# Kernel optimization log

Hardware: AMD Instinct MI355X
Metric: run time of the kernel (lower is better)

The kernel has to match this reference:

```python
import jax, jax.numpy as jnp
import numpy as np

STRICT_MAXIMA_BONUS = 10.0
FINAL_ADJUSTMENT = 0.0


def setup_inputs() -> dict:
    key = jax.random.key(0)
    x = jax.random.normal(key, (2, 8, 4, 256, 384), dtype=jnp.float32)
    return {"x": x}


def _conv_quad_interp3d(x, bonus, adj):
    B, C, D, H, W = x.shape
    # replicate ('edge') padding of 1 voxel, as kornia spatial_gradient3d does
    xp = jnp.pad(x, ((0, 0), (0, 0), (1, 1), (1, 1), (1, 1)), mode='edge')

    def f(dd, dh, dw):  # shifted view: value at (d+dd, h+dh, w+dw)
        return xp[:, :, 1 + dd:1 + dd + D, 1 + dh:1 + dh + H, 1 + dw:1 + dw + W]

    # first-order gradients (kornia diff kernels; depth kernel is flipped -> ds has sign of f(d-1)-f(d+1))
    b0 = 0.5 * (f(0, 0, 1) - f(0, 0, -1))   # dx
    b1 = 0.5 * (f(0, 1, 0) - f(0, -1, 0))   # dy
    b2 = 0.5 * (f(-1, 0, 0) - f(1, 0, 0))   # ds (flipped depth)

    # second-order (Hessian) entries; mixed terms carry the caller's 0.25 factor
    dxx = f(0, 0, 1) - 2.0 * x + f(0, 0, -1)
    dyy = f(0, 1, 0) - 2.0 * x + f(0, -1, 0)
    dss = f(1, 0, 0) - 2.0 * x + f(-1, 0, 0)
    dxy = 0.25 * (f(0, -1, -1) - f(0, -1, 1) - f(0, 1, -1) + f(0, 1, 1))
    dys = 0.25 * (-f(-1, -1, 0) + f(-1, 1, 0) + f(1, -1, 0) - f(1, 1, 0))  # depth-flipped
    dxs = 0.25 * (-f(-1, 0, -1) + f(-1, 0, 1) + f(1, 0, -1) - f(1, 0, 1))  # depth-flipped

    # 3x3x3 NMS mask (max-pool with -inf padding, equality with center)
    mx = jax.lax.reduce_window(x, -jnp.inf, jax.lax.max,
                               (1, 1, 3, 3, 3), (1, 1, 1, 1, 1), 'SAME')
    nms = x == mx

    # closed-form symmetric 3x3 solve: Hes @ u = b via adjugate / det
    # Hes = [[dxx,dxy,dxs],[dxy,dyy,dys],[dxs,dys,dss]]
    c00 = dyy * dss - dys * dys
    c01 = dxs * dys - dxy * dss
    c02 = dxy * dys - dxs * dyy
    c11 = dxx * dss - dxs * dxs
    c12 = dxy * dxs - dxx * dys
    c22 = dxx * dyy - dxy * dxy
    det = dxx * c00 + dxy * c01 + dxs * c02
    ok = nms & (det != 0)                       # new_nms_mask (solved correctly)
    invdet = 1.0 / jnp.where(det == 0, 1.0, det)
    u0 = (c00 * b0 + c01 * b1 + c02 * b2) * invdet
    u1 = (c01 * b0 + c11 * b1 + c12 * b2) * invdet
    u2 = (c02 * b0 + c12 * b1 + c22 * b2) * invdet

    # dx = -x_solved, only at valid NMS positions
    d0 = jnp.where(ok, -u0, 0.0)
    d1 = jnp.where(ok, -u1, 0.0)
    d2 = jnp.where(ok, -u2, 0.0)
    # zero out offsets with max-abs component > 0.7
    small = jnp.maximum(jnp.maximum(jnp.abs(d0), jnp.abs(d1)), jnp.abs(d2)) <= 0.7
    d0 = jnp.where(small, d0, 0.0)
    d1 = jnp.where(small, d1, 0.0)
    d2 = jnp.where(small, d2, 0.0)

    # quadratic value refinement dy = 0.5 * b^T dx, plus strict-maxima bonus
    dE = 0.5 * (b0 * d0 + b1 * d1 + b2 * d2)
    y_max = x + dE + bonus * ok.astype(x.dtype)

    # coords: grid channels are (d, x=w, y=h); dx_res after flip+swap_xy is (s, x, y),
    # with final_adjustment added to the x,y channels
    gd = jnp.arange(D, dtype=x.dtype)[:, None, None]
    gw = jnp.arange(W, dtype=x.dtype)[None, None, :]
    gh = jnp.arange(H, dtype=x.dtype)[None, :, None]
    coords_max = jnp.stack([gd + d2, gw + (d0 + adj), gh + (d1 + adj)], axis=2)  # (B,C,3,D,H,W)
    return coords_max, y_max


def reference(x):
    return _conv_quad_interp3d(x, STRICT_MAXIMA_BONUS, FINAL_ADJUSTMENT)
```

## Files before the change

kernel.cpp:

```cpp
#include <hip/hip_runtime.h>

#define BB 2
#define CC 8
#define DD 4
#define HH 256
#define WW 384
#define WV 4
#define WT (WW / WV)

__global__ __launch_bounds__(256) void cqi3d_kernel(const float* __restrict__ x,
                                                    float* __restrict__ coords,
                                                    float* __restrict__ ymax) {
    const int tid = blockIdx.x * blockDim.x + threadIdx.x;
    const int nthreads = BB * CC * HH * WT;
    if (tid >= nthreads) return;

    const int wt = tid % WT;
    int t = tid / WT;
    const int h = t % HH;
    const int bc = t / HH;

    const int w0 = wt * WV;

    const int hm = h > 0 ? h - 1 : 0;
    const int hp = h < HH - 1 ? h + 1 : HH - 1;
    const int hr[3] = {hm, h, hp};
    const int wl = w0 > 0 ? w0 - 1 : 0;
    const int wr = (w0 + WV < WW) ? w0 + WV : WW - 1;

    float rb[DD][3][WV + 2];
#pragma unroll
    for (int p = 0; p < DD; ++p) {
#pragma unroll
        for (int j = 0; j < 3; ++j) {
            const float* row = x + (((size_t)bc * DD + p) * HH + hr[j]) * WW;
            const float4 v4 = *reinterpret_cast<const float4*>(row + w0);
            rb[p][j][1] = v4.x;
            rb[p][j][2] = v4.y;
            rb[p][j][3] = v4.z;
            rb[p][j][4] = v4.w;
            rb[p][j][0] = row[wl];
            rb[p][j][5] = row[wr];
        }
    }

    float vm[DD][WV + 2];
#pragma unroll
    for (int p = 0; p < DD; ++p)
#pragma unroll
        for (int xx = 0; xx < WV + 2; ++xx)
            vm[p][xx] = fmaxf(fmaxf(rb[p][0][xx], rb[p][1][xx]), rb[p][2][xx]);

    const size_t plane = (size_t)HH * WW;

#pragma unroll
    for (int d = 0; d < DD; ++d) {
        const int i0 = d > 0 ? d - 1 : 0;
        const int i1 = d;
        const int i2 = d < DD - 1 ? d + 1 : DD - 1;

        float dm[WV + 2];
#pragma unroll
        for (int xx = 0; xx < WV + 2; ++xx)
            dm[xx] = fmaxf(fmaxf(vm[i0][xx], vm[i1][xx]), vm[i2][xx]);

        float yv[WV], o0[WV], o1[WV], o2[WV];
#pragma unroll
        for (int kk = 0; kk < WV; ++kk) {
            const int q = kk + 1;
            const float c = rb[i1][1][q];

            const float b0 = 0.5f * (rb[i1][1][q + 1] - rb[i1][1][q - 1]);
            const float b1 = 0.5f * (rb[i1][2][q] - rb[i1][0][q]);
            const float b2 = 0.5f * (rb[i0][1][q] - rb[i2][1][q]);

            const float dxx = rb[i1][1][q + 1] - 2.0f * c + rb[i1][1][q - 1];
            const float dyy = rb[i1][2][q] - 2.0f * c + rb[i1][0][q];
            const float dss = rb[i2][1][q] - 2.0f * c + rb[i0][1][q];
            const float dxy = 0.25f * (rb[i1][0][q - 1] - rb[i1][0][q + 1] -
                                       rb[i1][2][q - 1] + rb[i1][2][q + 1]);
            const float dys = 0.25f * (-rb[i0][0][q] + rb[i0][2][q] +
                                       rb[i2][0][q] - rb[i2][2][q]);
            const float dxs = 0.25f * (-rb[i0][1][q - 1] + rb[i0][1][q + 1] +
                                       rb[i2][1][q - 1] - rb[i2][1][q + 1]);

            const float mx = fmaxf(fmaxf(dm[q - 1], dm[q]), dm[q + 1]);
            const bool nms = (c == mx);

            const float c00 = dyy * dss - dys * dys;
            const float c01 = dxs * dys - dxy * dss;
            const float c02 = dxy * dys - dxs * dyy;
            const float c11 = dxx * dss - dxs * dxs;
            const float c12 = dxy * dxs - dxx * dys;
            const float c22 = dxx * dyy - dxy * dxy;
            const float det = dxx * c00 + dxy * c01 + dxs * c02;

            const bool ok = nms && (det != 0.0f);
            const float invdet = 1.0f / (det == 0.0f ? 1.0f : det);
            const float u0 = (c00 * b0 + c01 * b1 + c02 * b2) * invdet;
            const float u1 = (c01 * b0 + c11 * b1 + c12 * b2) * invdet;
            const float u2 = (c02 * b0 + c12 * b1 + c22 * b2) * invdet;

            float d0 = ok ? -u0 : 0.0f;
            float d1 = ok ? -u1 : 0.0f;
            float d2 = ok ? -u2 : 0.0f;

            const bool small = fmaxf(fmaxf(fabsf(d0), fabsf(d1)), fabsf(d2)) <= 0.7f;
            if (!small) { d0 = 0.0f; d1 = 0.0f; d2 = 0.0f; }

            const float dE = 0.5f * (b0 * d0 + b1 * d1 + b2 * d2);
            yv[kk] = c + dE + (ok ? 10.0f : 0.0f);
            o2[kk] = (float)d + d2;
            o0[kk] = (float)(w0 + kk) + d0;
            o1[kk] = (float)h + d1;
        }

        const size_t ybase = (((size_t)bc * DD + d) * HH + h) * WW + w0;
        *reinterpret_cast<float4*>(ymax + ybase) = make_float4(yv[0], yv[1], yv[2], yv[3]);

        const size_t cbase = (((size_t)bc * 3) * DD + d) * plane + (size_t)h * WW + w0;
        *reinterpret_cast<float4*>(coords + cbase) =
            make_float4(o2[0], o2[1], o2[2], o2[3]);
        *reinterpret_cast<float4*>(coords + cbase + DD * plane) =
            make_float4(o0[0], o0[1], o0[2], o0[3]);
        *reinterpret_cast<float4*>(coords + cbase + 2 * DD * plane) =
            make_float4(o1[0], o1[1], o1[2], o1[3]);
    }
}

extern "C" void kernel_launch(void* const* d_in, const int* in_sizes, int n_in,
                              void* d_out, int out_size, void* d_ws, size_t ws_size,
                              hipStream_t stream) {
    const float* x = (const float*)d_in[0];
    float* out = (float*)d_out;
    float* coords = out;
    float* ymax = out + (size_t)BB * CC * 3 * DD * HH * WW;

    const int nthreads = BB * CC * HH * WT;
    const int block = 256;
    const int grid = (nthreads + block - 1) / block;
    cqi3d_kernel<<<grid, block, 0, stream>>>(x, coords, ymax);
}
```

Before: 28.34 us.

## Split depth across threads and use nontemporal vector stores

Each thread now handles one depth slice instead of looping over all four, so the launch has four times as many threads, each loading only the three neighbouring depth planes. This cuts per-thread register use and raises parallelism, in exchange for reloading overlapping planes (9 row loads per output slice instead of 12 shared across 4 slices). Output stores become nontemporal vector stores so the write-only outputs bypass cache retention.

```diff
diff --git a/kernel.cpp b/kernel.cpp
--- a/kernel.cpp
+++ b/kernel.cpp
@@ -8,124 +8,119 @@
 #define WV 4
 #define WT (WW / WV)
 
+typedef float f32x4 __attribute__((ext_vector_type(4)));
+
 __global__ __launch_bounds__(256) void cqi3d_kernel(const float* __restrict__ x,
                                                     float* __restrict__ coords,
                                                     float* __restrict__ ymax) {
     const int tid = blockIdx.x * blockDim.x + threadIdx.x;
-    const int nthreads = BB * CC * HH * WT;
+    const int nthreads = BB * CC * DD * HH * WT;
     if (tid >= nthreads) return;
 
     const int wt = tid % WT;
     int t = tid / WT;
     const int h = t % HH;
-    const int bc = t / HH;
+    t /= HH;
+    const int d = t % DD;
+    const int bc = t / DD;
 
     const int w0 = wt * WV;
 
     const int hm = h > 0 ? h - 1 : 0;
     const int hp = h < HH - 1 ? h + 1 : HH - 1;
     const int hr[3] = {hm, h, hp};
+    const int dpl[3] = {d > 0 ? d - 1 : 0, d, d < DD - 1 ? d + 1 : DD - 1};
     const int wl = w0 > 0 ? w0 - 1 : 0;
     const int wr = (w0 + WV < WW) ? w0 + WV : WW - 1;
 
-    float rb[DD][3][WV + 2];
+    float rb[3][3][WV + 2];
 #pragma unroll
-    for (int p = 0; p < DD; ++p) {
+    for (int i = 0; i < 3; ++i) {
 #pragma unroll
         for (int j = 0; j < 3; ++j) {
-            const float* row = x + (((size_t)bc * DD + p) * HH + hr[j]) * WW;
-            const float4 v4 = *reinterpret_cast<const float4*>(row + w0);
-            rb[p][j][1] = v4.x;
-            rb[p][j][2] = v4.y;
-            rb[p][j][3] = v4.z;
-            rb[p][j][4] = v4.w;
-            rb[p][j][0] = row[wl];
-            rb[p][j][5] = row[wr];
+            const float* row = x + (((size_t)bc * DD + dpl[i]) * HH + hr[j]) * WW;
+            const f32x4 v4 = *reinterpret_cast<const f32x4*>(row + w0);
+            rb[i][j][1] = v4.x;
+            rb[i][j][2] = v4.y;
+            rb[i][j][3] = v4.z;
+            rb[i][j][4] = v4.w;
+            rb[i][j][0] = row[wl];
+            rb[i][j][5] = row[wr];
         }
     }
 
-    float vm[DD][WV + 2];
+    float dm[WV + 2];
 #pragma unroll
-    for (int p = 0; p < DD; ++p)
+    for (int xx = 0; xx < WV + 2; ++xx) {
+        const float m0 = fmaxf(fmaxf(rb[0][0][xx], rb[0][1][xx]), rb[0][2][xx]);
+        const float m1 = fmaxf(fmaxf(rb[1][0][xx], rb[1][1][xx]), rb[1][2][xx]);
+        const float m2 = fmaxf(fmaxf(rb[2][0][xx], rb[2][1][xx]), rb[2][2][xx]);
+        dm[xx] = fmaxf(fmaxf(m0, m1), m2);
+    }
+
+    float yv[WV], o0[WV], o1[WV], o2[WV];
 #pragma unroll
-        for (int xx = 0; xx < WV + 2; ++xx)
-            vm[p][xx] = fmaxf(fmaxf(rb[p][0][xx], rb[p][1][xx]), rb[p][2][xx]);
+    for (int kk = 0; kk < WV; ++kk) {
+        const int q = kk + 1;
+        const float c = rb[1][1][q];
+
+        const float b0 = 0.5f * (rb[1][1][q + 1] - rb[1][1][q - 1]);
+        const float b1 = 0.5f * (rb[1][2][q] - rb[1][0][q]);
+        const float b2 = 0.5f * (rb[0][1][q] - rb[2][1][q]);
+
+        const float dxx = rb[1][1][q + 1] - 2.0f * c + rb[1][1][q - 1];
+        const float dyy = rb[1][2][q] - 2.0f * c + rb[1][0][q];
+        const float dss = rb[2][1][q] - 2.0f * c + rb[0][1][q];
+        const float dxy = 0.25f * (rb[1][0][q - 1] - rb[1][0][q + 1] -
+                                   rb[1][2][q - 1] + rb[1][2][q + 1]);
+        const float dys = 0.25f * (-rb[0][0][q] + rb[0][2][q] +
+                                   rb[2][0][q] - rb[2][2][q]);
+        const float dxs = 0.25f * (-rb[0][1][q - 1] + rb[0][1][q + 1] +
+                                   rb[2][1][q - 1] - rb[2][1][q + 1]);
+
+        const float mx = fmaxf(fmaxf(dm[q - 1], dm[q]), dm[q + 1]);
+        const bool nms = (c == mx);
+
+        const float c00 = dyy * dss - dys * dys;
+        const float c01 = dxs * dys - dxy * dss;
+        const float c02 = dxy * dys - dxs * dyy;
+        const float c11 = dxx * dss - dxs * dxs;
+        const float c12 = dxy * dxs - dxx * dys;
+        const float c22 = dxx * dyy - dxy * dxy;
+        const float det = dxx * c00 + dxy * c01 + dxs * c02;
+
+        const bool ok = nms && (det != 0.0f);
+        const float invdet = 1.0f / (det == 0.0f ? 1.0f : det);
+        const float u0 = (c00 * b0 + c01 * b1 + c02 * b2) * invdet;
+        const float u1 = (c01 * b0 + c11 * b1 + c12 * b2) * invdet;
+        const float u2 = (c02 * b0 + c12 * b1 + c22 * b2) * invdet;
+
+        float d0 = ok ? -u0 : 0.0f;
+        float d1 = ok ? -u1 : 0.0f;
+        float d2 = ok ? -u2 : 0.0f;
+
+        const bool small = fmaxf(fmaxf(fabsf(d0), fabsf(d1)), fabsf(d2)) <= 0.7f;
+        if (!small) { d0 = 0.0f; d1 = 0.0f; d2 = 0.0f; }
+
+        const float dE = 0.5f * (b0 * d0 + b1 * d1 + b2 * d2);
+        yv[kk] = c + dE + (ok ? 10.0f : 0.0f);
+        o2[kk] = (float)d + d2;
+        o0[kk] = (float)(w0 + kk) + d0;
+        o1[kk] = (float)h + d1;
+    }
 
     const size_t plane = (size_t)HH * WW;
+    const size_t ybase = (((size_t)bc * DD + d) * HH + h) * WW + w0;
+    const f32x4 yq = {yv[0], yv[1], yv[2], yv[3]};
+    __builtin_nontemporal_store(yq, reinterpret_cast<f32x4*>(ymax + ybase));
 
-#pragma unroll
-    for (int d = 0; d < DD; ++d) {
-        const int i0 = d > 0 ? d - 1 : 0;
-        const int i1 = d;
-        const int i2 = d < DD - 1 ? d + 1 : DD - 1;
-
-        float dm[WV + 2];
-#pragma unroll
-        for (int xx = 0; xx < WV + 2; ++xx)
-            dm[xx] = fmaxf(fmaxf(vm[i0][xx], vm[i1][xx]), vm[i2][xx]);
-
-        float yv[WV], o0[WV], o1[WV], o2[WV];
-#pragma unroll
-        for (int kk = 0; kk < WV; ++kk) {
-            const int q = kk + 1;
-            const float c = rb[i1][1][q];
-
-            const float b0 = 0.5f * (rb[i1][1][q + 1] - rb[i1][1][q - 1]);
-            const float b1 = 0.5f * (rb[i1][2][q] - rb[i1][0][q]);
-            const float b2 = 0.5f * (rb[i0][1][q] - rb[i2][1][q]);
-
-            const float dxx = rb[i1][1][q + 1] - 2.0f * c + rb[i1][1][q - 1];
-            const float dyy = rb[i1][2][q] - 2.0f * c + rb[i1][0][q];
-            const float dss = rb[i2][1][q] - 2.0f * c + rb[i0][1][q];
-            const float dxy = 0.25f * (rb[i1][0][q - 1] - rb[i1][0][q + 1] -
-                                       rb[i1][2][q - 1] + rb[i1][2][q + 1]);
-            const float dys = 0.25f * (-rb[i0][0][q] + rb[i0][2][q] +
-                                       rb[i2][0][q] - rb[i2][2][q]);
-            const float dxs = 0.25f * (-rb[i0][1][q - 1] + rb[i0][1][q + 1] +
-                                       rb[i2][1][q - 1] - rb[i2][1][q + 1]);
-
-            const float mx = fmaxf(fmaxf(dm[q - 1], dm[q]), dm[q + 1]);
-            const bool nms = (c == mx);
-
-            const float c00 = dyy * dss - dys * dys;
-            const float c01 = dxs * dys - dxy * dss;
-            const float c02 = dxy * dys - dxs * dyy;
-            const float c11 = dxx * dss - dxs * dxs;
-            const float c12 = dxy * dxs - dxx * dys;
-            const float c22 = dxx * dyy - dxy * dxy;
-            const float det = dxx * c00 + dxy * c01 + dxs * c02;
-
-            const bool ok = nms && (det != 0.0f);
-            const float invdet = 1.0f / (det == 0.0f ? 1.0f : det);
-            const float u0 = (c00 * b0 + c01 * b1 + c02 * b2) * invdet;
-            const float u1 = (c01 * b0 + c11 * b1 + c12 * b2) * invdet;
-            const float u2 = (c02 * b0 + c12 * b1 + c22 * b2) * invdet;
-
-            float d0 = ok ? -u0 : 0.0f;
-            float d1 = ok ? -u1 : 0.0f;
-            float d2 = ok ? -u2 : 0.0f;
-
-            const bool small = fmaxf(fmaxf(fabsf(d0), fabsf(d1)), fabsf(d2)) <= 0.7f;
-            if (!small) { d0 = 0.0f; d1 = 0.0f; d2 = 0.0f; }
-
-            const float dE = 0.5f * (b0 * d0 + b1 * d1 + b2 * d2);
-            yv[kk] = c + dE + (ok ? 10.0f : 0.0f);
-            o2[kk] = (float)d + d2;
-            o0[kk] = (float)(w0 + kk) + d0;
-            o1[kk] = (float)h + d1;
-        }
-
-        const size_t ybase = (((size_t)bc * DD + d) * HH + h) * WW + w0;
-        *reinterpret_cast<float4*>(ymax + ybase) = make_float4(yv[0], yv[1], yv[2], yv[3]);
-
-        const size_t cbase = (((size_t)bc * 3) * DD + d) * plane + (size_t)h * WW + w0;
-        *reinterpret_cast<float4*>(coords + cbase) =
-            make_float4(o2[0], o2[1], o2[2], o2[3]);
-        *reinterpret_cast<float4*>(coords + cbase + DD * plane) =
-            make_float4(o0[0], o0[1], o0[2], o0[3]);
-        *reinterpret_cast<float4*>(coords + cbase + 2 * DD * plane) =
-            make_float4(o1[0], o1[1], o1[2], o1[3]);
-    }
+    const size_t cbase = (((size_t)bc * 3) * DD + d) * plane + (size_t)h * WW + w0;
+    const f32x4 q2 = {o2[0], o2[1], o2[2], o2[3]};
+    const f32x4 q0 = {o0[0], o0[1], o0[2], o0[3]};
+    const f32x4 q1 = {o1[0], o1[1], o1[2], o1[3]};
+    __builtin_nontemporal_store(q2, reinterpret_cast<f32x4*>(coords + cbase));
+    __builtin_nontemporal_store(q0, reinterpret_cast<f32x4*>(coords + cbase + DD * plane));
+    __builtin_nontemporal_store(q1, reinterpret_cast<f32x4*>(coords + cbase + 2 * DD * plane));
 }
 
 extern "C" void kernel_launch(void* const* d_in, const int* in_sizes, int n_in,
@@ -136,7 +131,7 @@
     float* coords = out;
     float* ymax = out + (size_t)BB * CC * 3 * DD * HH * WW;
 
-    const int nthreads = BB * CC * HH * WT;
+    const int nthreads = BB * CC * DD * HH * WT;
     const int block = 256;
     const int grid = (nthreads + block - 1) / block;
     cqi3d_kernel<<<grid, block, 0, stream>>>(x, coords, ymax);
```

After: 41.04 us. 44.8% more time.
